# Kernel optimization log

Hardware: AMD Instinct MI355X
Metric: run time of the kernel (lower is better)

## Reference

```python
import jax, jax.numpy as jnp
import numpy as np
from jax import lax

NMS_SIZE = 5
THR = 0.0
B, C, H, W = 8, 1, 2048, 2048
# fixed capacity for the jit-compatible nonzero (padded with -1); generous upper
# bound on number of surviving local maxima (~HW/25 per map, half above thr=0)
MAX_KEYPOINTS = 2_000_000


def setup_inputs() -> dict:
    key = jax.random.key(0)
    scores = jax.random.normal(key, (B, C, H, W), dtype=jnp.float32)
    return {"scores": scores}


def _local_max(scores):
    # MaxPool2d(kernel=5, stride=1, padding=2) == SAME-padded windowed max
    return lax.reduce_window(
        scores,
        -jnp.inf,
        lax.max,
        window_dimensions=(1, 1, NMS_SIZE, NMS_SIZE),
        window_strides=(1, 1, 1, 1),
        padding="SAME",
    )


def reference(scores):
    maxima = (scores == _local_max(scores)) & (scores > THR)  # [B,C,H,W] bool
    # torch: maxima.nonzero().t()[2:4] -> (row, col) coordinates of survivors.
    # jit-compatible fixed-size nonzero, padded with -1 (extra entries beyond
    # the true count are fill values, matching a compacted index list).
    _, _, hh, ww = jnp.nonzero(maxima, size=MAX_KEYPOINTS, fill_value=-1)
    return jnp.stack([hh, ww])  # [2, MAX_KEYPOINTS] int
```

## Files before the change

kernel.cpp:

```cpp
#include <hip/hip_runtime.h>
#include <stdint.h>
#include <math.h>

#define BATCH 8
#define HH 2048
#define WW 2048
#define NTOT (BATCH * HH * WW)
#define NWORDS (NTOT / 32)
#define R 16
#define NSTRIPS (HH / R)
#define NBLK (NSTRIPS * BATCH)
#define BLK_WORDS (R * WW / 32)
#define MAXK 2000000

__global__ __launch_bounds__(256) void nms_mask(const float* __restrict__ scores,
                                                uint8_t* __restrict__ maskbytes,
                                                int* __restrict__ counts) {
    const int strip = blockIdx.x;
    const int b     = blockIdx.y;
    const int tid   = threadIdx.x;
    const int lane  = tid & 63;
    const int wv    = tid >> 6;
    const int c0    = wv * 512 + lane * 8;
    const int h0    = strip * R;
    const float* img  = scores + (size_t)b * HH * WW;
    const float* colp = img + c0;

    const bool has_l = (c0 != 0);
    const bool has_r = (c0 != WW - 8);

    float win[5][12];

#define LOAD_ROW(PH, hrow)                                                    \
    do {                                                                      \
        const int h_ = (hrow);                                                \
        if ((unsigned)h_ < (unsigned)HH) {                                    \
            const float* p_ = colp + (size_t)h_ * WW;                         \
            float4 a_ = *(const float4*)(p_);                                 \
            float4 b_ = *(const float4*)(p_ + 4);                             \
            win[PH][2] = a_.x; win[PH][3] = a_.y;                             \
            win[PH][4] = a_.z; win[PH][5] = a_.w;                             \
            win[PH][6] = b_.x; win[PH][7] = b_.y;                             \
            win[PH][8] = b_.z; win[PH][9] = b_.w;                             \
            if (has_l) {                                                      \
                float2 hl_ = *(const float2*)(p_ - 2);                        \
                win[PH][0] = hl_.x; win[PH][1] = hl_.y;                       \
            } else { win[PH][0] = -INFINITY; win[PH][1] = -INFINITY; }        \
            if (has_r) {                                                      \
                float2 hr_ = *(const float2*)(p_ + 8);                        \
                win[PH][10] = hr_.x; win[PH][11] = hr_.y;                     \
            } else { win[PH][10] = -INFINITY; win[PH][11] = -INFINITY; }      \
        } else {                                                              \
            _Pragma("unroll")                                                 \
            for (int k_ = 0; k_ < 12; ++k_) win[PH][k_] = -INFINITY;          \
        }                                                                     \
    } while (0)

    LOAD_ROW(0, h0 - 2);
    LOAD_ROW(1, h0 - 1);
    LOAD_ROW(2, h0 + 0);
    LOAD_ROW(3, h0 + 1);

    int pc = 0;
    size_t outbyte = (((size_t)(b * HH + h0) * WW) + c0) >> 3;

#pragma unroll
    for (int i = 0; i < R; ++i) {
        LOAD_ROW((4 + i) % 5, h0 + 2 + i);
        const int CEN = (2 + i) % 5;

        float v[12];
#pragma unroll
        for (int k = 0; k < 12; ++k)
            v[k] = fmaxf(fmaxf(fmaxf(win[0][k], win[1][k]),
                               fmaxf(win[2][k], win[3][k])), win[4][k]);
        float p[11];
#pragma unroll
        for (int k = 0; k < 11; ++k) p[k] = fmaxf(v[k], v[k + 1]);

        uint32_t byte = 0;
#pragma unroll
        for (int j = 0; j < 8; ++j) {
            const float hm = fmaxf(fmaxf(p[j], p[j + 2]), v[j + 4]);
            const float s  = win[CEN][j + 2];
            if ((s == hm) && (s > 0.0f)) byte |= (1u << j);
        }
        maskbytes[outbyte] = (uint8_t)byte;
        outbyte += WW / 8;
        pc += __popc(byte);
    }
#undef LOAD_ROW

#pragma unroll
    for (int d = 32; d >= 1; d >>= 1) pc += __shfl_down(pc, d, 64);
    __shared__ int wsum[4];
    if (lane == 0) wsum[wv] = pc;
    __syncthreads();
    if (tid == 0) counts[b * NSTRIPS + strip] = wsum[0] + wsum[1] + wsum[2] + wsum[3];
}

__global__ void scan_counts(const int* __restrict__ counts, int* __restrict__ offsets) {
    const int lane = threadIdx.x;
    int local[16];
    int sum = 0;
#pragma unroll
    for (int i = 0; i < 16; ++i) {
        local[i] = counts[lane * 16 + i];
        sum += local[i];
    }
    int incl = sum;
#pragma unroll
    for (int d = 1; d < 64; d <<= 1) {
        int n = __shfl_up(incl, d, 64);
        if (lane >= d) incl += n;
    }
    int excl = incl - sum;
#pragma unroll
    for (int i = 0; i < 16; ++i) {
        offsets[lane * 16 + i] = excl;
        excl += local[i];
    }
    if (lane == 63) offsets[NBLK] = incl;
}

__global__ __launch_bounds__(256) void tail_fill(const int* __restrict__ total_p,
                                                 int* __restrict__ out_h,
                                                 int* __restrict__ out_w) {
    int total = *total_p;
    if (total < 0) total = 0;
    if (total > MAXK) total = MAXK;

    const int base = (blockIdx.x * 256 + threadIdx.x) * 4;
    if (base >= MAXK) return;
    if (base + 4 <= total) return;

    if (base >= total) {
        const int4 neg = make_int4(-1, -1, -1, -1);
        *(int4*)(out_h + base) = neg;
        *(int4*)(out_w + base) = neg;
    } else {
#pragma unroll
        for (int j = 0; j < 4; ++j) {
            const int idx = base + j;
            if (idx >= total) { out_h[idx] = -1; out_w[idx] = -1; }
        }
    }
}

__global__ __launch_bounds__(256) void compact(const uint32_t* __restrict__ bitmask,
                                               const int* __restrict__ offsets,
                                               int* __restrict__ out_h,
                                               int* __restrict__ out_w) {
    const int chunk = blockIdx.x;
    const int tid = threadIdx.x;
    const uint32_t* base = bitmask + (size_t)chunk * BLK_WORDS;
    uint4 m = ((const uint4*)base)[tid];
    uint32_t words[4] = {m.x, m.y, m.z, m.w};
    int pc = __popc(m.x) + __popc(m.y) + __popc(m.z) + __popc(m.w);

    const int lane = tid & 63, wv = tid >> 6;
    int incl = pc;
#pragma unroll
    for (int d = 1; d < 64; d <<= 1) {
        int n = __shfl_up(incl, d, 64);
        if (lane >= d) incl += n;
    }
    __shared__ int wsums[4];
    if (lane == 63) wsums[wv] = incl;
    __syncthreads();
    int wbase = 0;
    for (int i = 0; i < wv; ++i) wbase += wsums[i];

    int off = offsets[chunk] + wbase + (incl - pc);

    uint32_t idx0 = ((uint32_t)chunk * BLK_WORDS + (uint32_t)tid * 4u) * 32u;
#pragma unroll
    for (int wj = 0; wj < 4; ++wj) {
        uint32_t mm = words[wj];
        const uint32_t ib = idx0 + (uint32_t)wj * 32u;
        while (mm) {
            const int bit = __ffs(mm) - 1;
            mm &= mm - 1;
            const uint32_t idx = ib + bit;
            if (off < MAXK) {
                out_h[off] = (int)((idx >> 11) & 2047);
                out_w[off] = (int)(idx & 2047);
            }
            ++off;
        }
    }
}

extern "C" void kernel_launch(void* const* d_in, const int* in_sizes, int n_in,
                              void* d_out, int out_size, void* d_ws, size_t ws_size,
                              hipStream_t stream) {
    const float* scores = (const float*)d_in[0];
    int* out = (int*)d_out;

    uint32_t* bitmask = (uint32_t*)d_ws;
    int* counts  = (int*)((char*)d_ws + (size_t)NWORDS * 4);
    int* offsets = counts + NBLK;

    nms_mask<<<dim3(NSTRIPS, BATCH), 256, 0, stream>>>(scores, (uint8_t*)bitmask, counts);
    scan_counts<<<1, 64, 0, stream>>>(counts, offsets);
    tail_fill<<<(MAXK / 4 + 255) / 256, 256, 0, stream>>>(offsets + NBLK, out, out + MAXK);
    compact<<<NBLK, 256, 0, stream>>>(bitmask, offsets, out, out + MAXK);
}
```

Before: 46.03 us.

## Fuse scan, tail-fill and compaction into a single kernel launch

```diff
diff --git a/kernel.cpp b/kernel.cpp
--- a/kernel.cpp
+++ b/kernel.cpp
@@ -12,6 +12,7 @@
 #define NBLK (NSTRIPS * BATCH)
 #define BLK_WORDS (R * WW / 32)
 #define MAXK 2000000
+#define TAILBLK ((MAXK / 4 + 255) / 256)
 
 __global__ __launch_bounds__(256) void nms_mask(const float* __restrict__ scores,
                                                 uint8_t* __restrict__ maskbytes,
@@ -99,60 +100,60 @@
     if (tid == 0) counts[b * NSTRIPS + strip] = wsum[0] + wsum[1] + wsum[2] + wsum[3];
 }
 
-__global__ void scan_counts(const int* __restrict__ counts, int* __restrict__ offsets) {
-    const int lane = threadIdx.x;
-    int local[16];
-    int sum = 0;
-#pragma unroll
-    for (int i = 0; i < 16; ++i) {
-        local[i] = counts[lane * 16 + i];
-        sum += local[i];
-    }
-    int incl = sum;
-#pragma unroll
-    for (int d = 1; d < 64; d <<= 1) {
-        int n = __shfl_up(incl, d, 64);
-        if (lane >= d) incl += n;
-    }
-    int excl = incl - sum;
-#pragma unroll
-    for (int i = 0; i < 16; ++i) {
-        offsets[lane * 16 + i] = excl;
-        excl += local[i];
-    }
-    if (lane == 63) offsets[NBLK] = incl;
-}
-
-__global__ __launch_bounds__(256) void tail_fill(const int* __restrict__ total_p,
-                                                 int* __restrict__ out_h,
-                                                 int* __restrict__ out_w) {
-    int total = *total_p;
-    if (total < 0) total = 0;
-    if (total > MAXK) total = MAXK;
-
-    const int base = (blockIdx.x * 256 + threadIdx.x) * 4;
-    if (base >= MAXK) return;
-    if (base + 4 <= total) return;
-
-    if (base >= total) {
-        const int4 neg = make_int4(-1, -1, -1, -1);
-        *(int4*)(out_h + base) = neg;
-        *(int4*)(out_w + base) = neg;
-    } else {
-#pragma unroll
-        for (int j = 0; j < 4; ++j) {
-            const int idx = base + j;
-            if (idx >= total) { out_h[idx] = -1; out_w[idx] = -1; }
+__device__ __forceinline__ int block_sum(int v, int tid) {
+    const int lane = tid & 63, wv = tid >> 6;
+#pragma unroll
+    for (int d = 32; d >= 1; d >>= 1) v += __shfl_down(v, d, 64);
+    __shared__ int ws[4];
+    __shared__ int res;
+    if (lane == 0) ws[wv] = v;
+    __syncthreads();
+    if (tid == 0) res = ws[0] + ws[1] + ws[2] + ws[3];
+    __syncthreads();
+    return res;
+}
+
+__global__ __launch_bounds__(256) void compact_tail(const uint32_t* __restrict__ bitmask,
+                                                    const int* __restrict__ counts,
+                                                    int* __restrict__ out_h,
+                                                    int* __restrict__ out_w) {
+    const int tid = threadIdx.x;
+
+    if (blockIdx.x >= NBLK) {
+        const uint4 c4 = ((const uint4*)counts)[tid];
+        int total = block_sum((int)(c4.x + c4.y + c4.z + c4.w), tid);
+        if (total < 0) total = 0;
+        if (total > MAXK) total = MAXK;
+
+        const int base = ((int)(blockIdx.x - NBLK) * 256 + tid) * 4;
+        if (base >= MAXK) return;
+        if (base + 4 <= total) return;
+
+        if (base >= total) {
+            const int4 neg = make_int4(-1, -1, -1, -1);
+            *(int4*)(out_h + base) = neg;
+            *(int4*)(out_w + base) = neg;
+        } else {
+#pragma unroll
+            for (int j = 0; j < 4; ++j) {
+                const int idx = base + j;
+                if (idx >= total) { out_h[idx] = -1; out_w[idx] = -1; }
+            }
         }
-    }
-}
-
-__global__ __launch_bounds__(256) void compact(const uint32_t* __restrict__ bitmask,
-                                               const int* __restrict__ offsets,
-                                               int* __restrict__ out_h,
-                                               int* __restrict__ out_w) {
+        return;
+    }
+
     const int chunk = blockIdx.x;
-    const int tid = threadIdx.x;
+
+    const uint4 c4 = ((const uint4*)counts)[tid];
+    const int i0 = tid * 4;
+    int contrib = 0;
+    contrib += (i0 + 0 < chunk) ? (int)c4.x : 0;
+    contrib += (i0 + 1 < chunk) ? (int)c4.y : 0;
+    contrib += (i0 + 2 < chunk) ? (int)c4.z : 0;
+    contrib += (i0 + 3 < chunk) ? (int)c4.w : 0;
+    const int chunk_base = block_sum(contrib, tid);
+
     const uint32_t* base = bitmask + (size_t)chunk * BLK_WORDS;
     uint4 m = ((const uint4*)base)[tid];
     uint32_t words[4] = {m.x, m.y, m.z, m.w};
@@ -171,7 +172,7 @@
     int wbase = 0;
     for (int i = 0; i < wv; ++i) wbase += wsums[i];
 
-    int off = offsets[chunk] + wbase + (incl - pc);
+    int off = chunk_base + wbase + (incl - pc);
 
     uint32_t idx0 = ((uint32_t)chunk * BLK_WORDS + (uint32_t)tid * 4u) * 32u;
 #pragma unroll
@@ -198,11 +199,8 @@
     int* out = (int*)d_out;
 
     uint32_t* bitmask = (uint32_t*)d_ws;
-    int* counts  = (int*)((char*)d_ws + (size_t)NWORDS * 4);
-    int* offsets = counts + NBLK;
+    int* counts = (int*)((char*)d_ws + (size_t)NWORDS * 4);
 
     nms_mask<<<dim3(NSTRIPS, BATCH), 256, 0, stream>>>(scores, (uint8_t*)bitmask, counts);
-    scan_counts<<<1, 64, 0, stream>>>(counts, offsets);
-    tail_fill<<<(MAXK / 4 + 255) / 256, 256, 0, stream>>>(offsets + NBLK, out, out + MAXK);
-    compact<<<NBLK, 256, 0, stream>>>(bitmask, offsets, out, out + MAXK);
-}
+    compact_tail<<<NBLK + TAILBLK, 256, 0, stream>>>(bitmask, counts, out, out + MAXK);
+}
```

Result: faster. 42.90 us (-6.8%).
